# Kernel optimization log

Measured on AMD Instinct MI355X. Metric: run time of the kernel, lower is better.

The kernel has to match this reference:

```python
import jax, jax.numpy as jnp
import numpy as np

N = 10000; E = 160000; NF = 5; EF = 3; H = 8; C = 128; HC = H * C; G = 16

def _glorot(key, shape):
    s = float(np.sqrt(6.0 / (shape[0] + shape[-1])))
    return jax.random.uniform(key, shape, minval=-s, maxval=s, dtype=jnp.float32)

def setup_inputs():
    key = jax.random.key(0)
    ks = jax.random.split(key, 32)
    inp = {}
    inp["x"] = jax.random.normal(ks[0], (N, NF), dtype=jnp.float32)
    inp["edge_index"] = jax.random.randint(ks[1], (2, E), 0, N, dtype=jnp.int32)
    inp["edge_attr"] = jax.random.normal(ks[2], (E, EF), dtype=jnp.float32)
    inp["batch"] = jnp.sort(jax.random.randint(ks[3], (N,), 0, G, dtype=jnp.int32))
    ins = [NF, HC, HC, HC]
    i = 4
    for l in range(4):
        inp[f"W{l+1}"] = _glorot(ks[i], (ins[l], HC)); i += 1
        inp[f"We{l+1}"] = _glorot(ks[i], (EF, HC)); i += 1
        inp[f"as{l+1}"] = _glorot(ks[i], (H, C)); i += 1
        inp[f"ad{l+1}"] = _glorot(ks[i], (H, C)); i += 1
        inp[f"ae{l+1}"] = _glorot(ks[i], (H, C)); i += 1
        inp[f"b{l+1}"] = jnp.zeros((HC if l < 3 else C,), jnp.float32)
    inp["lin_w"] = _glorot(ks[i], (C, 1)) * 2.0
    inp["lin_b"] = jnp.zeros((1,), jnp.float32)
    return inp

def _gat(x, src, dst, ea, W, We, a_s, a_d, a_e, bias, concat):
    # PyG GATConv with edge_dim, add_self_loops=True, fill_value='mean'
    n = x.shape[0]
    cnt = jax.ops.segment_sum(jnp.ones((src.shape[0],), x.dtype), dst, n)
    loop_attr = jax.ops.segment_sum(ea, dst, n) / jnp.maximum(cnt, 1.0)[:, None]
    sl = jnp.arange(n, dtype=src.dtype)
    src2 = jnp.concatenate([src, sl])
    dst2 = jnp.concatenate([dst, sl])
    ea2 = jnp.concatenate([ea, loop_attr], axis=0)
    xl = (x @ W).reshape(n, H, C)                       # [N,H,C]
    a_src = jnp.einsum("nhc,hc->nh", xl, a_s)
    a_dst = jnp.einsum("nhc,hc->nh", xl, a_d)
    el = (ea2 @ We).reshape(-1, H, C)                    # [E2,H,C]
    alpha = a_src[src2] + a_dst[dst2] + jnp.einsum("ehc,hc->eh", el, a_e)
    alpha = jax.nn.leaky_relu(alpha, 0.2)
    m = jax.ops.segment_max(alpha, dst2, n)
    m = jnp.where(jnp.isfinite(m), m, 0.0)
    ex = jnp.exp(alpha - m[dst2])
    den = jax.ops.segment_sum(ex, dst2, n)
    alpha = ex / (den[dst2] + 1e-16)                     # segment softmax over dst
    out = jax.ops.segment_sum(alpha[:, :, None] * xl[src2], dst2, n)  # [N,H,C]
    if concat:
        return out.reshape(n, HC) + bias
    return out.mean(axis=1) + bias

def reference(x, edge_index, edge_attr, batch,
              W1, We1, as1, ad1, ae1, b1,
              W2, We2, as2, ad2, ae2, b2,
              W3, We3, as3, ad3, ae3, b3,
              W4, We4, as4, ad4, ae4, b4,
              lin_w, lin_b):
    src, dst = edge_index[0], edge_index[1]
    h = jax.nn.elu(_gat(x, src, dst, edge_attr, W1, We1, as1, ad1, ae1, b1, True))
    h = jax.nn.elu(_gat(h, src, dst, edge_attr, W2, We2, as2, ad2, ae2, b2, True))
    h = jax.nn.elu(_gat(h, src, dst, edge_attr, W3, We3, as3, ad3, ae3, b3, True))
    h = jax.nn.elu(_gat(h, src, dst, edge_attr, W4, We4, as4, ad4, ae4, b4, False))
    cnt = jax.ops.segment_sum(jnp.ones((N,), h.dtype), batch, G)
    pooled = jax.ops.segment_sum(h, batch, G) / jnp.maximum(cnt, 1.0)[:, None]
    return (pooled @ lin_w + lin_b).squeeze(-1)
```

## Files before the change

### kernel.cpp

```cpp
#include <hip/hip_runtime.h>
#include <math.h>

#define Nn 10000
#define En 160000
#define NF 5
#define EF 3
#define Hh 8
#define Cc 128
#define HC 1024
#define Gg 16

#define Mpad 10112

typedef __attribute__((ext_vector_type(8))) _Float16 half8;
typedef __attribute__((ext_vector_type(4))) float f32x4;


__device__ __forceinline__ void gl_lds16(const void* g, void* l) {
    __builtin_amdgcn_global_load_lds((const __attribute__((address_space(1))) void*)g,
                                     (__attribute__((address_space(3))) void*)l, 16, 0, 0);
}

__device__ __forceinline__ float elu_f(float v) {
    return (v > 0.f) ? v : expm1f(v);
}


__global__ void deg_sum_k(const int* __restrict__ dst, const float* __restrict__ ea,
                          int* __restrict__ cnt, float* __restrict__ sum_ea) {
    int e = blockIdx.x * 256 + threadIdx.x;
    if (e >= En) return;
    int d = dst[e];
    atomicAdd(&cnt[d], 1);
    atomicAdd(&sum_ea[d * 3 + 0], ea[e * 3 + 0]);
    atomicAdd(&sum_ea[d * 3 + 1], ea[e * 3 + 1]);
    atomicAdd(&sum_ea[d * 3 + 2], ea[e * 3 + 2]);
}

__global__ void finish_loop_k(const int* __restrict__ cnt, float* __restrict__ loop_attr) {
    int n = blockIdx.x * 256 + threadIdx.x;
    if (n >= Nn) return;
    float s = 1.0f / fmaxf((float)cnt[n], 1.0f);
    loop_attr[n * 3 + 0] *= s;
    loop_attr[n * 3 + 1] *= s;
    loop_attr[n * 3 + 2] *= s;
}

__global__ __launch_bounds__(1024) void scan_k(const int* __restrict__ cnt,
                                               int* __restrict__ rowptr,
                                               int* __restrict__ fillptr) {
    __shared__ int sh[1024];
    int tid = threadIdx.x;
    int base = 0;
    for (int chunk = 0; chunk < Nn; chunk += 1024) {
        int i = chunk + tid;
        int v = (i < Nn) ? cnt[i] : 0;
        sh[tid] = v;
        __syncthreads();
        for (int off = 1; off < 1024; off <<= 1) {
            int t = (tid >= off) ? sh[tid - off] : 0;
            __syncthreads();
            sh[tid] += t;
            __syncthreads();
        }
        int excl = sh[tid] - v;
        if (i < Nn) { rowptr[i] = base + excl; fillptr[i] = base + excl; }
        int total = sh[1023];
        __syncthreads();
        base += total;
    }
    if (tid == 0) rowptr[Nn] = base;
}

__global__ void csr_fill_k(const int* __restrict__ src, const int* __restrict__ dst,
                           int* __restrict__ fillptr, int* __restrict__ epos,
                           int* __restrict__ srcP) {
    int e = blockIdx.x * 256 + threadIdx.x;
    if (e >= En) return;
    int d = dst[e];
    int pos = atomicAdd(&fillptr[d], 1);
    epos[e] = pos;
    srcP[pos] = src[e];
}

__global__ void bounds_k(const int* __restrict__ batch, int* __restrict__ gstart) {
    int i = blockIdx.x * 256 + threadIdx.x;
    if (i >= Nn) return;
    int b = batch[i];
    if (i == 0) {
        for (int g = 0; g <= b; ++g) gstart[g] = 0;
    } else {
        int pb = batch[i - 1];
        for (int g = pb + 1; g <= b; ++g) gstart[g] = i;
    }
    if (i == Nn - 1) {
        for (int g = b + 1; g <= Gg; ++g) gstart[g] = Nn;
    }
}


__global__ void wae_all_k(const float* __restrict__ We1, const float* __restrict__ ae1,
                          const float* __restrict__ We2, const float* __restrict__ ae2,
                          const float* __restrict__ We3, const float* __restrict__ ae3,
                          const float* __restrict__ We4, const float* __restrict__ ae4,
                          float* __restrict__ w_ae_all) {
    int t = threadIdx.x;
    if (t >= 96) return;
    int l = t / 24, idx = t % 24;
    int f = idx >> 3, h = idx & 7;
    const float* We = (l == 0) ? We1 : (l == 1) ? We2 : (l == 2) ? We3 : We4;
    const float* ae = (l == 0) ? ae1 : (l == 1) ? ae2 : (l == 2) ? ae3 : ae4;
    float s = 0.f;
    for (int c = 0; c < Cc; ++c) s += We[f * HC + h * Cc + c] * ae[h * Cc + c];
    w_ae_all[l * 24 + f * 8 + h] = s;
}

__global__ __launch_bounds__(1024) void wsplit_all_k(const float* __restrict__ W2,
                                                     const float* __restrict__ W3,
                                                     const float* __restrict__ W4,
                                                     _Float16* __restrict__ Wt16) {
    __shared__ float tile[32][33];
    int z = blockIdx.z;
    const float* W = (z == 0) ? W2 : (z == 1) ? W3 : W4;
    int nb = blockIdx.x * 32, kb = blockIdx.y * 32;
    tile[threadIdx.y][threadIdx.x] = W[(size_t)(kb + threadIdx.y) * HC + nb + threadIdx.x];
    __syncthreads();
    float x = tile[threadIdx.x][threadIdx.y];
    int n = nb + threadIdx.y, k = kb + threadIdx.x;
    Wt16[(size_t)z * HC * HC + (size_t)n * HC + k] = (_Float16)x;
}


__global__ void gemm_k5(const float* __restrict__ x, const float* __restrict__ Wm,
                        _Float16* __restrict__ out16) {
    int n = blockIdx.x;
    int tid = threadIdx.x;
    __shared__ float xr[8];
    if (tid < NF) xr[tid] = x[n * NF + tid];
    __syncthreads();
    float x0 = xr[0], x1 = xr[1], x2 = xr[2], x3 = xr[3], x4 = xr[4];
    for (int j = tid; j < HC; j += 256) {
        float v = x0 * Wm[j] + x1 * Wm[HC + j] + x2 * Wm[2 * HC + j]
                + x3 * Wm[3 * HC + j] + x4 * Wm[4 * HC + j];
        out16[(size_t)n * HC + j] = (_Float16)v;
    }
}

__global__ __launch_bounds__(256) void gemm_mfma(const _Float16* __restrict__ A,
                                                 const _Float16* __restrict__ Bt,
                                                 _Float16* __restrict__ C16) {
    __shared__ _Float16 As[128 * 32];
    __shared__ _Float16 Bs[128 * 32];
    int tid = threadIdx.x;
    int wave = tid >> 6, lane = tid & 63;
    int wr = wave >> 1, wc = wave & 1;
    int row0 = blockIdx.y * 128;
    int col0 = blockIdx.x * 128;

    f32x4 acc[4][4];
#pragma unroll
    for (int i = 0; i < 4; ++i)
#pragma unroll
        for (int j = 0; j < 4; ++j) acc[i][j] = (f32x4){0.f, 0.f, 0.f, 0.f};

    int srow = lane >> 2;
    int scol = (lane & 3) * 8;
    int fr = lane & 15;
    int fk = (lane >> 4) * 8;

    for (int kb = 0; kb < 1024; kb += 32) {
#pragma unroll
        for (int cc = 0; cc < 2; ++cc) {
            int c = wave + cc * 4;
            int r = c * 16 + srow;
            gl_lds16(A + (size_t)(row0 + r) * 1024 + kb + scol, &As[c * 512 + lane * 8]);
            gl_lds16(Bt + (size_t)(col0 + r) * 1024 + kb + scol, &Bs[c * 512 + lane * 8]);
        }
        __syncthreads();

        half8 af[4], bf[4];
#pragma unroll
        for (int i = 0; i < 4; ++i)
            af[i] = *(const half8*)&As[(wr * 64 + i * 16 + fr) * 32 + fk];
#pragma unroll
        for (int j = 0; j < 4; ++j)
            bf[j] = *(const half8*)&Bs[(wc * 64 + j * 16 + fr) * 32 + fk];
#pragma unroll
        for (int i = 0; i < 4; ++i)
#pragma unroll
            for (int j = 0; j < 4; ++j)
                acc[i][j] = __builtin_amdgcn_mfma_f32_16x16x32_f16(af[i], bf[j], acc[i][j],
                                                                   0, 0, 0);
        __syncthreads();
    }

    int cn = lane & 15, rq = (lane >> 4) * 4;
#pragma unroll
    for (int i = 0; i < 4; ++i) {
        int rbase = row0 + wr * 64 + i * 16 + rq;
#pragma unroll
        for (int j = 0; j < 4; ++j) {
            int col = col0 + wc * 64 + j * 16 + cn;
#pragma unroll
            for (int r = 0; r < 4; ++r) {
                int row = rbase + r;
                if (row < Nn) C16[(size_t)row * HC + col] = (_Float16)acc[i][j][r];
            }
        }
    }
}


__global__ __launch_bounds__(256) void attn_nodes_k(const _Float16* __restrict__ xl16,
                                                    const float* __restrict__ a_s,
                                                    const float* __restrict__ a_d,
                                                    float* __restrict__ a_src,
                                                    float* __restrict__ a_dst) {
    int wid = (blockIdx.x * 256 + threadIdx.x) >> 6;
    int lane = threadIdx.x & 63;
    if (wid >= Nn * Hh) return;
    int n = wid >> 3, h = wid & 7;
    const _Float16* row = xl16 + (size_t)n * HC + h * Cc;
    float c0 = (float)row[lane * 2], c1 = (float)row[lane * 2 + 1];
    float2 sv = *(const float2*)&a_s[h * Cc + lane * 2];
    float2 dv = *(const float2*)&a_d[h * Cc + lane * 2];
    float s1 = c0 * sv.x + c1 * sv.y;
    float s2 = c0 * dv.x + c1 * dv.y;
#pragma unroll
    for (int off = 32; off; off >>= 1) {
        s1 += __shfl_xor(s1, off);
        s2 += __shfl_xor(s2, off);
    }
    if (lane == 0) { a_src[wid] = s1; a_dst[wid] = s2; }
}

__global__ void alpha_edge_k(const int* __restrict__ src, const int* __restrict__ dst,
                             const int* __restrict__ epos, const float* __restrict__ ea,
                             const float* __restrict__ a_src, const float* __restrict__ a_dst,
                             const float* __restrict__ w_ae, float* __restrict__ alphaP) {
    int e = blockIdx.x * 256 + threadIdx.x;
    if (e >= En) return;
    int s = src[e], d = dst[e];
    int pos = epos[e];
    float f0 = ea[e * 3 + 0], f1 = ea[e * 3 + 1], f2 = ea[e * 3 + 2];
#pragma unroll
    for (int h = 0; h < Hh; ++h) {
        float v = a_src[s * Hh + h] + a_dst[d * Hh + h]
                + f0 * w_ae[h] + f1 * w_ae[Hh + h] + f2 * w_ae[2 * Hh + h];
        alphaP[(size_t)pos * Hh + h] = (v > 0.f) ? v : 0.2f * v;
    }
}

__global__ __launch_bounds__(256) void aggregate_k(const _Float16* __restrict__ xl16,
                                                   const float* __restrict__ alphaP,
                                                   const float* __restrict__ loop_attr,
                                                   const float* __restrict__ a_srcB,
                                                   const float* __restrict__ a_dstB,
                                                   const float* __restrict__ w_ae,
                                                   const int* __restrict__ rowptr,
                                                   const int* __restrict__ srcP,
                                                   const float* __restrict__ bias,
                                                   const float* __restrict__ lin_w,
                                                   _Float16* __restrict__ A2,
                                                   float* __restrict__ dnode,
                                                   int raw_mode) {
    int n = (blockIdx.x * 256 + threadIdx.x) >> 6;
    int lane = threadIdx.x & 63;
    if (n >= Nn) return;
    int beg = rowptr[n], end = rowptr[n + 1];
    int hh = lane & 7;
    int slot = lane >> 3;
    int hc = lane >> 3;

    float f0 = loop_attr[n * 3 + 0], f1 = loop_attr[n * 3 + 1], f2 = loop_attr[n * 3 + 2];
    float av = a_srcB[n * 8 + hh] + a_dstB[n * 8 + hh]
             + f0 * w_ae[hh] + f1 * w_ae[8 + hh] + f2 * w_ae[16 + hh];
    float aself = (av > 0.f) ? av : 0.2f * av;

    float m = (slot == 0) ? aself : -3.0e38f;
    float s = (slot == 0) ? 1.0f : 0.0f;
    for (int i = beg + slot; i < end; i += 8) {
        float a = alphaP[(size_t)i * 8 + hh];
        if (a > m) { s = s * __expf(m - a) + 1.0f; m = a; }
        else s += __expf(a - m);
    }
#pragma unroll
    for (int off = 8; off < 64; off <<= 1) {
        float mo = __shfl_xor(m, off);
        float so = __shfl_xor(s, off);
        float M = fmaxf(m, mo);
        s = s * __expf(m - M) + so * __expf(mo - M);
        m = M;
    }
    float inv = 1.f / (s + 1e-16f);
    float wself = __expf(aself - m) * inv;

    float m_c = __shfl(m, hc);
    float inv_c = __shfl(inv, hc);
    float wself_c = __shfl(wself, hc);

    float acc[16];
    {
        const _Float16* r = xl16 + (size_t)n * HC + lane * 16;
        half8 r0 = *(const half8*)r;
        half8 r1 = *(const half8*)(r + 8);
#pragma unroll
        for (int j = 0; j < 8; ++j) {
            acc[j] = wself_c * (float)r0[j];
            acc[8 + j] = wself_c * (float)r1[j];
        }
    }
    int loff = lane * 16;
    for (int i0 = beg; i0 < end; i0 += 4) {
        int last = end - 1;
        int i1 = (i0 + 1 < end) ? i0 + 1 : last;
        int i2 = (i0 + 2 < end) ? i0 + 2 : last;
        int i3 = (i0 + 3 < end) ? i0 + 3 : last;
        int s0 = srcP[i0], s1 = srcP[i1], s2 = srcP[i2], s3 = srcP[i3];
        float a0 = alphaP[(size_t)i0 * 8 + hc];
        float a1 = (i0 + 1 < end) ? alphaP[(size_t)i1 * 8 + hc] : -3.0e38f;
        float a2 = (i0 + 2 < end) ? alphaP[(size_t)i2 * 8 + hc] : -3.0e38f;
        float a3 = (i0 + 3 < end) ? alphaP[(size_t)i3 * 8 + hc] : -3.0e38f;
        const _Float16* p0 = xl16 + (size_t)s0 * HC + loff;
        const _Float16* p1 = xl16 + (size_t)s1 * HC + loff;
        const _Float16* p2 = xl16 + (size_t)s2 * HC + loff;
        const _Float16* p3 = xl16 + (size_t)s3 * HC + loff;
        half8 q0a = *(const half8*)p0, q0b = *(const half8*)(p0 + 8);
        half8 q1a = *(const half8*)p1, q1b = *(const half8*)(p1 + 8);
        half8 q2a = *(const half8*)p2, q2b = *(const half8*)(p2 + 8);
        half8 q3a = *(const half8*)p3, q3b = *(const half8*)(p3 + 8);
        float w0 = __expf(a0 - m_c) * inv_c;
        float w1 = __expf(a1 - m_c) * inv_c;
        float w2 = __expf(a2 - m_c) * inv_c;
        float w3 = __expf(a3 - m_c) * inv_c;
#pragma unroll
        for (int j = 0; j < 8; ++j) {
            float t0 = acc[j], t1 = acc[8 + j];
            t0 = fmaf(w0, (float)q0a[j], t0);  t1 = fmaf(w0, (float)q0b[j], t1);
            t0 = fmaf(w1, (float)q1a[j], t0);  t1 = fmaf(w1, (float)q1b[j], t1);
            t0 = fmaf(w2, (float)q2a[j], t0);  t1 = fmaf(w2, (float)q2b[j], t1);
            t0 = fmaf(w3, (float)q3a[j], t0);  t1 = fmaf(w3, (float)q3b[j], t1);
            acc[j] = t0; acc[8 + j] = t1;
        }
    }

    if (!raw_mode) {
        int ch = lane * 16;
        half8 hv0, hv1;
#pragma unroll
        for (int j = 0; j < 8; ++j) {
            hv0[j] = (_Float16)elu_f(acc[j] + bias[ch + j]);
            hv1[j] = (_Float16)elu_f(acc[8 + j] + bias[ch + 8 + j]);
        }
        _Float16* p = A2 + (size_t)n * 1024 + ch;
        *(half8*)p = hv0;
        *(half8*)(p + 8) = hv1;
    } else {
#pragma unroll
        for (int off = 8; off < 64; off <<= 1)
#pragma unroll
            for (int j = 0; j < 16; ++j) acc[j] += __shfl_xor(acc[j], off);
        int c0 = (lane & 7) * 16;
        float partial = 0.f;
#pragma unroll
        for (int j = 0; j < 16; ++j) {
            float v = elu_f(acc[j] * 0.125f + bias[c0 + j]);
            partial = fmaf(v, lin_w[c0 + j], partial);
        }
#pragma unroll
        for (int off = 1; off < 8; off <<= 1) partial += __shfl_xor(partial, off);
        if (lane == 0) dnode[n] = partial;
    }
}


__global__ __launch_bounds__(256) void pool_final_k(const float* __restrict__ dnode,
                                                    const int* __restrict__ gstart,
                                                    const float* __restrict__ lin_b,
                                                    float* __restrict__ out) {
    __shared__ float sh[256];
    int g = blockIdx.x;
    int tid = threadIdx.x;
    int s = gstart[g], e = gstart[g + 1];
    float acc = 0.f;
    for (int n = s + tid; n < e; n += 256) acc += dnode[n];
    sh[tid] = acc;
    __syncthreads();
    for (int off = 128; off; off >>= 1) {
        if (tid < off) sh[tid] += sh[tid + off];
        __syncthreads();
    }
    if (tid == 0) out[g] = sh[0] / fmaxf((float)(e - s), 1.f) + lin_b[0];
}


extern "C" void kernel_launch(void* const* d_in, const int* in_sizes, int n_in,
                              void* d_out, int out_size, void* d_ws, size_t ws_size,
                              hipStream_t stream) {
    const float* x = (const float*)d_in[0];
    const int* ei = (const int*)d_in[1];
    const float* ea = (const float*)d_in[2];
    const int* batch = (const int*)d_in[3];
    const float *Wl[4], *Wel[4], *asl[4], *adl[4], *ael[4], *bl[4];
    for (int l = 0; l < 4; ++l) {
        Wl[l] = (const float*)d_in[4 + 6 * l];
        Wel[l] = (const float*)d_in[5 + 6 * l];
        asl[l] = (const float*)d_in[6 + 6 * l];
        adl[l] = (const float*)d_in[7 + 6 * l];
        ael[l] = (const float*)d_in[8 + 6 * l];
        bl[l] = (const float*)d_in[9 + 6 * l];
    }
    const float* lin_w = (const float*)d_in[28];
    const float* lin_b = (const float*)d_in[29];
    const int* srcA = ei;
    const int* dstA = ei + En;

    float* Wp = (float*)d_ws;
    size_t o = 0;
    _Float16* A2 = (_Float16*)(Wp + o); o += (size_t)Mpad * 512;
    _Float16* Wt16 = (_Float16*)(Wp + o); o += (size_t)3 * HC * HC / 2;
    _Float16* xl16 = (_Float16*)(Wp + o); o += (size_t)Nn * HC / 2;
    float* alphaP = Wp + o; o += (size_t)En * Hh;
    float* loop_attr = Wp + o; o += Nn * 3;
    int* cnt = (int*)(Wp + o); o += Nn;
    int* rowptr = (int*)(Wp + o); o += Nn + 1;
    int* fillptr = (int*)(Wp + o); o += Nn;
    int* epos = (int*)(Wp + o); o += En;
    int* srcP = (int*)(Wp + o); o += En;
    int* gstart = (int*)(Wp + o); o += Gg + 1;
    float* a_srcB = Wp + o; o += Nn * Hh;
    float* a_dstB = Wp + o; o += Nn * Hh;
    float* w_ae_all = Wp + o; o += 128;
    float* dnode = Wp + o; o += Nn;

    hipMemsetAsync(cnt, 0, Nn * sizeof(int), stream);
    hipMemsetAsync(loop_attr, 0, Nn * 3 * sizeof(float), stream);

    deg_sum_k<<<(En + 255) / 256, 256, 0, stream>>>(dstA, ea, cnt, loop_attr);
    finish_loop_k<<<(Nn + 255) / 256, 256, 0, stream>>>(cnt, loop_attr);
    scan_k<<<1, 1024, 0, stream>>>(cnt, rowptr, fillptr);
    csr_fill_k<<<(En + 255) / 256, 256, 0, stream>>>(srcA, dstA, fillptr, epos, srcP);
    bounds_k<<<(Nn + 255) / 256, 256, 0, stream>>>(batch, gstart);
    wae_all_k<<<1, 128, 0, stream>>>(Wel[0], ael[0], Wel[1], ael[1], Wel[2], ael[2],
                                     Wel[3], ael[3], w_ae_all);
    wsplit_all_k<<<dim3(32, 32, 3), dim3(32, 32), 0, stream>>>(Wl[1], Wl[2], Wl[3], Wt16);

    for (int l = 0; l < 4; ++l) {
        if (l == 0)
            gemm_k5<<<Nn, 256, 0, stream>>>(x, Wl[0], xl16);
        else
            gemm_mfma<<<dim3(HC / 128, Mpad / 128), 256, 0, stream>>>(
                A2, Wt16 + (size_t)(l - 1) * HC * HC, xl16);
        attn_nodes_k<<<(Nn * Hh) / 4, 256, 0, stream>>>(xl16, asl[l], adl[l], a_srcB, a_dstB);
        alpha_edge_k<<<(En + 255) / 256, 256, 0, stream>>>(srcA, dstA, epos, ea, a_srcB,
                                                           a_dstB, w_ae_all + l * 24, alphaP);
        aggregate_k<<<(Nn + 3) / 4, 256, 0, stream>>>(xl16, alphaP, loop_attr, a_srcB,
                                                      a_dstB, w_ae_all + l * 24, rowptr,
                                                      srcP, bl[l], lin_w, A2, dnode,
                                                      (l == 3) ? 1 : 0);
    }
    pool_final_k<<<Gg, 256, 0, stream>>>(dnode, gstart, lin_b, (float*)d_out);
}
```

Before: 642.0 us.

## Fuse attention-score dot products into GEMM epilogue and compute edge logits in aggregate

Computes the per-node a_src/a_dst attention dot products in the GEMM epilogues (MFMA and first-layer kernels), using shuffle and LDS reductions over the fp32 accumulators. This removes the attn_nodes kernel. The alpha_edge kernel and its alphaP buffer are also dropped: edge logits are recomputed inside aggregate from a_src gathers and edge attributes permuted into CSR order as float4. This saves two launches per layer and the alphaP round trip, but adds recomputation and extra gathers in both aggregate passes, and the dot products now use fp32 values rather than fp16-rounded ones.

```diff
diff --git a/kernel.cpp b/kernel.cpp
--- a/kernel.cpp
+++ b/kernel.cpp
@@ -73,14 +73,14 @@
 }
 
 __global__ void csr_fill_k(const int* __restrict__ src, const int* __restrict__ dst,
-                           int* __restrict__ fillptr, int* __restrict__ epos,
-                           int* __restrict__ srcP) {
+                           const float* __restrict__ ea, int* __restrict__ fillptr,
+                           int* __restrict__ srcP, float4* __restrict__ eaP) {
     int e = blockIdx.x * 256 + threadIdx.x;
     if (e >= En) return;
     int d = dst[e];
     int pos = atomicAdd(&fillptr[d], 1);
-    epos[e] = pos;
     srcP[pos] = src[e];
+    eaP[pos] = make_float4(ea[e * 3 + 0], ea[e * 3 + 1], ea[e * 3 + 2], 0.f);
 }
 
 __global__ void bounds_k(const int* __restrict__ batch, int* __restrict__ gstart) {
@@ -132,10 +132,13 @@
 
 
 __global__ void gemm_k5(const float* __restrict__ x, const float* __restrict__ Wm,
-                        _Float16* __restrict__ out16) {
+                        const float* __restrict__ a_s, const float* __restrict__ a_d,
+                        _Float16* __restrict__ out16,
+                        float* __restrict__ a_srcB, float* __restrict__ a_dstB) {
     int n = blockIdx.x;
     int tid = threadIdx.x;
     __shared__ float xr[8];
+    __shared__ float vrow[HC];
     if (tid < NF) xr[tid] = x[n * NF + tid];
     __syncthreads();
     float x0 = xr[0], x1 = xr[1], x2 = xr[2], x3 = xr[3], x4 = xr[4];
@@ -143,19 +146,42 @@
         float v = x0 * Wm[j] + x1 * Wm[HC + j] + x2 * Wm[2 * HC + j]
                 + x3 * Wm[3 * HC + j] + x4 * Wm[4 * HC + j];
         out16[(size_t)n * HC + j] = (_Float16)v;
+        vrow[j] = v;
+    }
+    __syncthreads();
+    int w = tid >> 6, lane = tid & 63;
+#pragma unroll
+    for (int q = 0; q < 2; ++q) {
+        int h = w * 2 + q;
+        float v0 = vrow[h * Cc + lane], v1 = vrow[h * Cc + 64 + lane];
+        float s1 = v0 * a_s[h * Cc + lane] + v1 * a_s[h * Cc + 64 + lane];
+        float s2 = v0 * a_d[h * Cc + lane] + v1 * a_d[h * Cc + 64 + lane];
+#pragma unroll
+        for (int off = 32; off; off >>= 1) {
+            s1 += __shfl_xor(s1, off);
+            s2 += __shfl_xor(s2, off);
+        }
+        if (lane == 0) { a_srcB[n * 8 + h] = s1; a_dstB[n * 8 + h] = s2; }
     }
 }
 
 __global__ __launch_bounds__(256) void gemm_mfma(const _Float16* __restrict__ A,
                                                  const _Float16* __restrict__ Bt,
-                                                 _Float16* __restrict__ C16) {
+                                                 const float* __restrict__ a_s,
+                                                 const float* __restrict__ a_d,
+                                                 _Float16* __restrict__ C16,
+                                                 float* __restrict__ a_srcB,
+                                                 float* __restrict__ a_dstB) {
     __shared__ _Float16 As[128 * 32];
     __shared__ _Float16 Bs[128 * 32];
+    __shared__ float ps[128][2];
+    __shared__ float pd[128][2];
     int tid = threadIdx.x;
     int wave = tid >> 6, lane = tid & 63;
     int wr = wave >> 1, wc = wave & 1;
     int row0 = blockIdx.y * 128;
     int col0 = blockIdx.x * 128;
+    int h = blockIdx.x;
 
     f32x4 acc[4][4];
 #pragma unroll
@@ -208,51 +234,45 @@
             }
         }
     }
-}
-
-
-__global__ __launch_bounds__(256) void attn_nodes_k(const _Float16* __restrict__ xl16,
-                                                    const float* __restrict__ a_s,
-                                                    const float* __restrict__ a_d,
-                                                    float* __restrict__ a_src,
-                                                    float* __restrict__ a_dst) {
-    int wid = (blockIdx.x * 256 + threadIdx.x) >> 6;
-    int lane = threadIdx.x & 63;
-    if (wid >= Nn * Hh) return;
-    int n = wid >> 3, h = wid & 7;
-    const _Float16* row = xl16 + (size_t)n * HC + h * Cc;
-    float c0 = (float)row[lane * 2], c1 = (float)row[lane * 2 + 1];
-    float2 sv = *(const float2*)&a_s[h * Cc + lane * 2];
-    float2 dv = *(const float2*)&a_d[h * Cc + lane * 2];
-    float s1 = c0 * sv.x + c1 * sv.y;
-    float s2 = c0 * dv.x + c1 * dv.y;
-#pragma unroll
-    for (int off = 32; off; off >>= 1) {
-        s1 += __shfl_xor(s1, off);
-        s2 += __shfl_xor(s2, off);
-    }
-    if (lane == 0) { a_src[wid] = s1; a_dst[wid] = s2; }
-}
-
-__global__ void alpha_edge_k(const int* __restrict__ src, const int* __restrict__ dst,
-                             const int* __restrict__ epos, const float* __restrict__ ea,
-                             const float* __restrict__ a_src, const float* __restrict__ a_dst,
-                             const float* __restrict__ w_ae, float* __restrict__ alphaP) {
-    int e = blockIdx.x * 256 + threadIdx.x;
-    if (e >= En) return;
-    int s = src[e], d = dst[e];
-    int pos = epos[e];
-    float f0 = ea[e * 3 + 0], f1 = ea[e * 3 + 1], f2 = ea[e * 3 + 2];
-#pragma unroll
-    for (int h = 0; h < Hh; ++h) {
-        float v = a_src[s * Hh + h] + a_dst[d * Hh + h]
-                + f0 * w_ae[h] + f1 * w_ae[Hh + h] + f2 * w_ae[2 * Hh + h];
-        alphaP[(size_t)pos * Hh + h] = (v > 0.f) ? v : 0.2f * v;
-    }
-}
+    float asv[4], adv[4];
+#pragma unroll
+    for (int j = 0; j < 4; ++j) {
+        int c = wc * 64 + j * 16 + cn;
+        asv[j] = a_s[h * Cc + c];
+        adv[j] = a_d[h * Cc + c];
+    }
+#pragma unroll
+    for (int i = 0; i < 4; ++i)
+#pragma unroll
+        for (int r = 0; r < 4; ++r) {
+            float rs = acc[i][0][r] * asv[0] + acc[i][1][r] * asv[1]
+                     + acc[i][2][r] * asv[2] + acc[i][3][r] * asv[3];
+            float rd = acc[i][0][r] * adv[0] + acc[i][1][r] * adv[1]
+                     + acc[i][2][r] * adv[2] + acc[i][3][r] * adv[3];
+#pragma unroll
+            for (int off = 1; off < 16; off <<= 1) {
+                rs += __shfl_xor(rs, off);
+                rd += __shfl_xor(rd, off);
+            }
+            if (cn == 0) {
+                int rib = wr * 64 + i * 16 + rq + r;
+                ps[rib][wc] = rs;
+                pd[rib][wc] = rd;
+            }
+        }
+    __syncthreads();
+    if (tid < 128) {
+        int row = row0 + tid;
+        if (row < Nn) {
+            a_srcB[row * 8 + h] = ps[tid][0] + ps[tid][1];
+            a_dstB[row * 8 + h] = pd[tid][0] + pd[tid][1];
+        }
+    }
+}
+
 
 __global__ __launch_bounds__(256) void aggregate_k(const _Float16* __restrict__ xl16,
-                                                   const float* __restrict__ alphaP,
+                                                   const float4* __restrict__ eaP,
                                                    const float* __restrict__ loop_attr,
                                                    const float* __restrict__ a_srcB,
                                                    const float* __restrict__ a_dstB,
@@ -272,15 +292,20 @@
     int slot = lane >> 3;
     int hc = lane >> 3;
 
+    float w0 = w_ae[hh], w1 = w_ae[8 + hh], w2 = w_ae[16 + hh];
+    float adst_n = a_dstB[n * 8 + hh];
+    float asrc_n = a_srcB[n * 8 + hh];
     float f0 = loop_attr[n * 3 + 0], f1 = loop_attr[n * 3 + 1], f2 = loop_attr[n * 3 + 2];
-    float av = a_srcB[n * 8 + hh] + a_dstB[n * 8 + hh]
-             + f0 * w_ae[hh] + f1 * w_ae[8 + hh] + f2 * w_ae[16 + hh];
+    float av = asrc_n + adst_n + f0 * w0 + f1 * w1 + f2 * w2;
     float aself = (av > 0.f) ? av : 0.2f * av;
 
     float m = (slot == 0) ? aself : -3.0e38f;
     float s = (slot == 0) ? 1.0f : 0.0f;
     for (int i = beg + slot; i < end; i += 8) {
-        float a = alphaP[(size_t)i * 8 + hh];
+        int sn = srcP[i];
+        float4 e4 = eaP[i];
+        float a = a_srcB[sn * 8 + hh] + adst_n + e4.x * w0 + e4.y * w1 + e4.z * w2;
+        a = (a > 0.f) ? a : 0.2f * a;
         if (a > m) { s = s * __expf(m - a) + 1.0f; m = a; }
         else s += __expf(a - m);
     }
@@ -298,6 +323,8 @@
     float m_c = __shfl(m, hc);
     float inv_c = __shfl(inv, hc);
     float wself_c = __shfl(wself, hc);
+    float adst_nc = __shfl(adst_n, hc);
+    float w0c = w_ae[hc], w1c = w_ae[8 + hc], w2c = w_ae[16 + hc];
 
     float acc[16];
     {
@@ -313,14 +340,14 @@
     int loff = lane * 16;
     for (int i0 = beg; i0 < end; i0 += 4) {
         int last = end - 1;
-        int i1 = (i0 + 1 < end) ? i0 + 1 : last;
-        int i2 = (i0 + 2 < end) ? i0 + 2 : last;
-        int i3 = (i0 + 3 < end) ? i0 + 3 : last;
+        bool v1 = (i0 + 1 < end), v2 = (i0 + 2 < end), v3 = (i0 + 3 < end);
+        int i1 = v1 ? i0 + 1 : last;
+        int i2 = v2 ? i0 + 2 : last;
+        int i3 = v3 ? i0 + 3 : last;
         int s0 = srcP[i0], s1 = srcP[i1], s2 = srcP[i2], s3 = srcP[i3];
-        float a0 = alphaP[(size_t)i0 * 8 + hc];
-        float a1 = (i0 + 1 < end) ? alphaP[(size_t)i1 * 8 + hc] : -3.0e38f;
-        float a2 = (i0 + 2 < end) ? alphaP[(size_t)i2 * 8 + hc] : -3.0e38f;
-        float a3 = (i0 + 3 < end) ? alphaP[(size_t)i3 * 8 + hc] : -3.0e38f;
+        float4 e0 = eaP[i0], e1 = eaP[i1], e2 = eaP[i2], e3 = eaP[i3];
+        float as0 = a_srcB[s0 * 8 + hc], as1 = a_srcB[s1 * 8 + hc];
+        float as2 = a_srcB[s2 * 8 + hc], as3 = a_srcB[s3 * 8 + hc];
         const _Float16* p0 = xl16 + (size_t)s0 * HC + loff;
         const _Float16* p1 = xl16 + (size_t)s1 * HC + loff;
         const _Float16* p2 = xl16 + (size_t)s2 * HC + loff;
@@ -329,17 +356,25 @@
         half8 q1a = *(const half8*)p1, q1b = *(const half8*)(p1 + 8);
         half8 q2a = *(const half8*)p2, q2b = *(const half8*)(p2 + 8);
         half8 q3a = *(const half8*)p3, q3b = *(const half8*)(p3 + 8);
-        float w0 = __expf(a0 - m_c) * inv_c;
-        float w1 = __expf(a1 - m_c) * inv_c;
-        float w2 = __expf(a2 - m_c) * inv_c;
-        float w3 = __expf(a3 - m_c) * inv_c;
+        float al0 = as0 + adst_nc + e0.x * w0c + e0.y * w1c + e0.z * w2c;
+        float al1 = as1 + adst_nc + e1.x * w0c + e1.y * w1c + e1.z * w2c;
+        float al2 = as2 + adst_nc + e2.x * w0c + e2.y * w1c + e2.z * w2c;
+        float al3 = as3 + adst_nc + e3.x * w0c + e3.y * w1c + e3.z * w2c;
+        al0 = (al0 > 0.f) ? al0 : 0.2f * al0;
+        al1 = v1 ? ((al1 > 0.f) ? al1 : 0.2f * al1) : -3.0e38f;
+        al2 = v2 ? ((al2 > 0.f) ? al2 : 0.2f * al2) : -3.0e38f;
+        al3 = v3 ? ((al3 > 0.f) ? al3 : 0.2f * al3) : -3.0e38f;
+        float u0 = __expf(al0 - m_c) * inv_c;
+        float u1 = __expf(al1 - m_c) * inv_c;
+        float u2 = __expf(al2 - m_c) * inv_c;
+        float u3 = __expf(al3 - m_c) * inv_c;
 #pragma unroll
         for (int j = 0; j < 8; ++j) {
             float t0 = acc[j], t1 = acc[8 + j];
-            t0 = fmaf(w0, (float)q0a[j], t0);  t1 = fmaf(w0, (float)q0b[j], t1);
-            t0 = fmaf(w1, (float)q1a[j], t0);  t1 = fmaf(w1, (float)q1b[j], t1);
-            t0 = fmaf(w2, (float)q2a[j], t0);  t1 = fmaf(w2, (float)q2b[j], t1);
-            t0 = fmaf(w3, (float)q3a[j], t0);  t1 = fmaf(w3, (float)q3b[j], t1);
+            t0 = fmaf(u0, (float)q0a[j], t0);  t1 = fmaf(u0, (float)q0b[j], t1);
+            t0 = fmaf(u1, (float)q1a[j], t0);  t1 = fmaf(u1, (float)q1b[j], t1);
+            t0 = fmaf(u2, (float)q2a[j], t0);  t1 = fmaf(u2, (float)q2b[j], t1);
+            t0 = fmaf(u3, (float)q3a[j], t0);  t1 = fmaf(u3, (float)q3b[j], t1);
             acc[j] = t0; acc[8 + j] = t1;
         }
     }
@@ -420,12 +455,11 @@
     _Float16* A2 = (_Float16*)(Wp + o); o += (size_t)Mpad * 512;
     _Float16* Wt16 = (_Float16*)(Wp + o); o += (size_t)3 * HC * HC / 2;
     _Float16* xl16 = (_Float16*)(Wp + o); o += (size_t)Nn * HC / 2;
-    float* alphaP = Wp + o; o += (size_t)En * Hh;
+    float4* eaP = (float4*)(Wp + o); o += (size_t)En * 4;
     float* loop_attr = Wp + o; o += Nn * 3;
     int* cnt = (int*)(Wp + o); o += Nn;
     int* rowptr = (int*)(Wp + o); o += Nn + 1;
     int* fillptr = (int*)(Wp + o); o += Nn;
-    int* epos = (int*)(Wp + o); o += En;
     int* srcP = (int*)(Wp + o); o += En;
     int* gstart = (int*)(Wp + o); o += Gg + 1;
     float* a_srcB = Wp + o; o += Nn * Hh;
@@ -439,7 +473,7 @@
     deg_sum_k<<<(En + 255) / 256, 256, 0, stream>>>(dstA, ea, cnt, loop_attr);
     finish_loop_k<<<(Nn + 255) / 256, 256, 0, stream>>>(cnt, loop_attr);
     scan_k<<<1, 1024, 0, stream>>>(cnt, rowptr, fillptr);
-    csr_fill_k<<<(En + 255) / 256, 256, 0, stream>>>(srcA, dstA, fillptr, epos, srcP);
+    csr_fill_k<<<(En + 255) / 256, 256, 0, stream>>>(srcA, dstA, ea, fillptr, srcP, eaP);
     bounds_k<<<(Nn + 255) / 256, 256, 0, stream>>>(batch, gstart);
     wae_all_k<<<1, 128, 0, stream>>>(Wel[0], ael[0], Wel[1], ael[1], Wel[2], ael[2],
                                      Wel[3], ael[3], w_ae_all);
@@ -447,14 +481,11 @@
 
     for (int l = 0; l < 4; ++l) {
         if (l == 0)
-            gemm_k5<<<Nn, 256, 0, stream>>>(x, Wl[0], xl16);
+            gemm_k5<<<Nn, 256, 0, stream>>>(x, Wl[0], asl[0], adl[0], xl16, a_srcB, a_dstB);
         else
             gemm_mfma<<<dim3(HC / 128, Mpad / 128), 256, 0, stream>>>(
-                A2, Wt16 + (size_t)(l - 1) * HC * HC, xl16);
-        attn_nodes_k<<<(Nn * Hh) / 4, 256, 0, stream>>>(xl16, asl[l], adl[l], a_srcB, a_dstB);
-        alpha_edge_k<<<(En + 255) / 256, 256, 0, stream>>>(srcA, dstA, epos, ea, a_srcB,
-                                                           a_dstB, w_ae_all + l * 24, alphaP);
-        aggregate_k<<<(Nn + 3) / 4, 256, 0, stream>>>(xl16, alphaP, loop_attr, a_srcB,
+                A2, Wt16 + (size_t)(l - 1) * HC * HC, asl[l], adl[l], xl16, a_srcB, a_dstB);
+        aggregate_k<<<(Nn + 3) / 4, 256, 0, stream>>>(xl16, eaP, loop_attr, a_srcB,
                                                       a_dstB, w_ae_all + l * 24, rowptr,
                                                       srcP, bl[l], lin_w, A2, dnode,
                                                       (l == 3) ? 1 : 0);
```

After: 599.0 us. -6.7%, faster.
